# Performance work log

Measured on AMD Instinct MI355X. Metric: run time of the kernel, lower is better.

## Reference

```python
import jax, jax.numpy as jnp
import numpy as np

M_HIST = 5        # Anderson history depth (m=5 in anderson_solver)
N_POWER = 20      # power iterations to estimate sigma for spectral_norm
REG = 1e-4        # Tikhonov regularization on the Anderson LS system
MAX_ITER = 25     # deq_max_iter


def _l2norm(x):
    return x / (jnp.linalg.norm(x) + 1e-12)


def spectral_normalize(W):
    # torch spectral_norm: W / sigma, sigma = u^T W v with u,v from power iteration
    u = _l2norm(jnp.ones((W.shape[0],), W.dtype))
    def body(_, u):
        v = _l2norm(W.T @ u)
        return _l2norm(W @ v)
    u = jax.lax.fori_loop(0, N_POWER, body, u)
    v = _l2norm(W.T @ u)
    u = jax.lax.stop_gradient(u)
    v = jax.lax.stop_gradient(v)
    sigma = u @ (W @ v)
    return W / sigma


def make_f(W1, b1, W2, b2):
    W1s = spectral_normalize(W1)
    W2s = spectral_normalize(W2)
    def f(z, context):
        h = jnp.tanh(jnp.concatenate([z, context], axis=-1) @ W1s.T + b1)
        return jnp.tanh(h @ W2s.T + b2)
    return f


def anderson(f, x0, context, max_iter, m=M_HIST):
    # Mirrors anderson_solver, including its duplicated warm-up step.
    X = [x0]
    F = [f(x0, context)]
    x = F[0]; X.append(x); F.append(f(x, context))
    x = F[0]; X.append(x); F.append(f(x, context))
    for _k in range(2, max_iter):
        m_k = min(len(X) - 1, m)
        dX = jnp.stack([X[-i] - X[-i - 1] for i in range(1, m_k + 1)], axis=-1)  # [B,d,mk]
        dF = jnp.stack([F[-i] - F[-i - 1] for i in range(1, m_k + 1)], axis=-1)
        dG = dF - dX
        A = jnp.einsum('bdi,bdj->bij', dG, dG) + REG * jnp.eye(m_k, dtype=x0.dtype)
        r = F[-1] - X[-1]
        Bv = jnp.einsum('bdi,bd->bi', dG, r)
        alpha = jnp.linalg.solve(A, Bv[..., None])[..., 0]          # [B,mk]
        x = F[-1] - jnp.einsum('bdi,bi->bd', dF, alpha)
        X.append(x)
        F.append(f(x, context))
        if len(X) > m + 1:
            X.pop(0); F.pop(0)
    return X[-1]


def setup_inputs() -> dict:
    key = jax.random.key(0)
    ks = jax.random.split(key, 5)
    B, X_DIM, LATENT, HIDDEN = 2048, 256, 256, 1024
    context = jax.random.normal(ks[0], (B, X_DIM), jnp.float32)
    W1 = jax.random.normal(ks[1], (HIDDEN, LATENT + X_DIM), jnp.float32) / np.sqrt(LATENT + X_DIM)
    b1 = jax.random.normal(ks[2], (HIDDEN,), jnp.float32) * 0.01
    W2 = jax.random.normal(ks[3], (LATENT, HIDDEN), jnp.float32) / np.sqrt(HIDDEN)
    b2 = jax.random.normal(ks[4], (LATENT,), jnp.float32) * 0.01
    return {"context": context, "W1": W1, "b1": b1, "W2": W2, "b2": b2}


def reference(context, W1, b1, W2, b2):
    f = make_f(W1, b1, W2, b2)
    z0 = jnp.zeros((context.shape[0], W2.shape[0]), context.dtype)
    z_star = anderson(f, z0, context, MAX_ITER)
    return z_star
```

## Files before the change

### kernel.cpp

```cpp
#include <hip/hip_runtime.h>
#include <hip/hip_bf16.h>


#define B_ROWS 2048
#define D_LAT  256
#define D_CTX  256
#define D_HID  1024
#define KCAT   512
#define SLOT   (B_ROWS * D_LAT)
#define NRING  7

typedef __bf16 bf16x8 __attribute__((ext_vector_type(8)));
typedef float f32x4 __attribute__((ext_vector_type(4)));
typedef unsigned short u16;

__global__ void init_kernel(const float* __restrict__ ctx,
                            __hip_bfloat16* __restrict__ zc,
                            float* __restrict__ vA, float* __restrict__ uA,
                            float* __restrict__ G1p, float* __restrict__ G2) {
  int i = blockIdx.x * 256 + threadIdx.x;
  if (i < B_ROWS * KCAT) {
    int b = i >> 9, c = i & 511;
    float v = (c < 256) ? 0.0f : ctx[b * 256 + (c - 256)];
    zc[i] = __float2bfloat16(v);
  }
  if (i < 512 * 512) G1p[i] = 0.0f;
  if (i < 256 * 256) G2[i] = 0.0f;
  if (i < KCAT) vA[i] = 0.0f;
  if (i < D_LAT) uA[i] = 1.0f;
}

__global__ __launch_bounds__(256) void gram_kernel(
    const float* __restrict__ W1, const float* __restrict__ W2,
    float* __restrict__ G1p, float* __restrict__ G2) {
  __shared__ float As[32][66];
  __shared__ float Bs[32][34];
  const int tid = threadIdx.x;
  const int tx = tid & 15, ty = tid >> 4;

  const float* X; float* G; int N, ti, tj, k0base; bool modeA;
  int b = blockIdx.x;
  if (b < 1024) {
    modeA = true; X = W1; G = G1p; N = 512;
    int s = b >> 7, t = b & 127;
    ti = t >> 4; tj = t & 15; k0base = s * 128;
  } else {
    modeA = false; b -= 1024; X = W2; G = G2; N = 256;
    int s = b >> 5, t = b & 31;
    ti = t >> 3; tj = t & 7; k0base = s * 128;
  }

  float acc[4][2] = {};
  for (int k0 = k0base; k0 < k0base + 128; k0 += 32) {
    if (modeA) {
      for (int idx = tid; idx < 2048; idx += 256) {
        int r = idx & 63, c = idx >> 6;
        As[c][r] = X[(size_t)(k0 + c) * 512 + ti * 64 + r];
      }
      for (int idx = tid; idx < 1024; idx += 256) {
        int r = idx & 31, c = idx >> 5;
        Bs[c][r] = X[(size_t)(k0 + c) * 512 + tj * 32 + r];
      }
    } else {
      for (int idx = tid; idx < 2048; idx += 256) {
        int c = idx & 31, r = idx >> 5;
        As[c][r] = X[(size_t)(ti * 64 + r) * 1024 + k0 + c];
      }
      for (int idx = tid; idx < 1024; idx += 256) {
        int c = idx & 31, r = idx >> 5;
        Bs[c][r] = X[(size_t)(tj * 32 + r) * 1024 + k0 + c];
      }
    }
    __syncthreads();
#pragma unroll
    for (int kk = 0; kk < 32; kk++) {
      const float2* ap = (const float2*)&As[kk][ty * 4];
      float2 a0 = ap[0], a1 = ap[1];
      float2 b0 = *(const float2*)&Bs[kk][tx * 2];
      float a[4] = {a0.x, a0.y, a1.x, a1.y};
      float bb[2] = {b0.x, b0.y};
#pragma unroll
      for (int i = 0; i < 4; i++)
#pragma unroll
        for (int j = 0; j < 2; j++) acc[i][j] += a[i] * bb[j];
    }
    __syncthreads();
  }
#pragma unroll
  for (int i = 0; i < 4; i++)
#pragma unroll
    for (int j = 0; j < 2; j++)
      atomicAdd(&G[(size_t)(ti * 64 + ty * 4 + i) * N + tj * 32 + tx * 2 + j],
                acc[i][j]);
}

__global__ __launch_bounds__(256) void colsum_kernel(
    const float* __restrict__ W1, float* __restrict__ vA) {
  int b = blockIdx.x;
  for (int c = threadIdx.x; c < KCAT; c += 256) {
    float s = 0.f;
#pragma unroll
    for (int r = 0; r < 16; r++) s += W1[(size_t)(16 * b + r) * KCAT + c];
    atomicAdd(&vA[c], s);
  }
}

__global__ __launch_bounds__(256) void pmv_kernel(
    const float* __restrict__ G1p, const float* __restrict__ G2,
    const float* __restrict__ vi, float* __restrict__ vo,
    const float* __restrict__ ui, float* __restrict__ uo, int g1_active) {
  int gw = blockIdx.x * 4 + (threadIdx.x >> 6);
  int lane = threadIdx.x & 63;
  const float* G; const float* in; float* out; int n, r;
  if (gw < 512) {
    if (!g1_active) return;
    G = G1p; in = vi; out = vo; n = 512; r = gw;
  } else {
    G = G2; in = ui; out = uo; n = 256; r = gw - 512;
  }
  const float4* Gr = (const float4*)(G + (size_t)r * n);
  const float4* uv = (const float4*)in;
  float acc = 0.f;
  for (int c = lane; c < (n >> 2); c += 64) {
    float4 g = Gr[c], u = uv[c];
    acc += g.x * u.x + g.y * u.y + g.z * u.z + g.w * u.w;
  }
  for (int off = 32; off; off >>= 1) acc += __shfl_down(acc, off, 64);
  if (lane == 0) out[r] = 0.25f * acc;
}

__global__ __launch_bounds__(256) void sigma_kernel(
    const float* __restrict__ vA, const float* __restrict__ vB,
    const float* __restrict__ uA, const float* __restrict__ uB,
    float* __restrict__ sig) {
  float s[4] = {0.f, 0.f, 0.f, 0.f};
  for (int i = threadIdx.x; i < KCAT; i += 256) {
    s[0] += vA[i] * vB[i];
    s[1] += vA[i] * vA[i];
  }
  for (int i = threadIdx.x; i < D_LAT; i += 256) {
    s[2] += uA[i] * uA[i];
    s[3] += uA[i] * uB[i];
  }
  __shared__ float red[4][4];
  int lane = threadIdx.x & 63, w = threadIdx.x >> 6;
  for (int k = 0; k < 4; k++) {
    float a = s[k];
    for (int off = 32; off; off >>= 1) a += __shfl_down(a, off, 64);
    if (lane == 0) red[k][w] = a;
  }
  __syncthreads();
  if (threadIdx.x == 0) {
    float d0 = red[0][0] + red[0][1] + red[0][2] + red[0][3];
    float d1 = red[1][0] + red[1][1] + red[1][2] + red[1][3];
    float d2 = red[2][0] + red[2][1] + red[2][2] + red[2][3];
    float d3 = red[3][0] + red[3][1] + red[3][2] + red[3][3];
    sig[0] = sqrtf(0.25f * d0 / d1);
    sig[1] = sqrtf(0.25f * d2 / d3);
  }
}

__global__ void wfold_kernel(const float* __restrict__ W1,
                             const float* __restrict__ W2,
                             const float* __restrict__ sig,
                             __hip_bfloat16* __restrict__ W1b,
                             __hip_bfloat16* __restrict__ W2b) {
  int i = blockIdx.x * 256 + threadIdx.x;
  if (i < D_HID * KCAT) W1b[i] = __float2bfloat16(W1[i] * sig[0]);
  int j = i - D_HID * KCAT;
  if (j >= 0 && j < D_LAT * D_HID) W2b[j] = __float2bfloat16(W2[j] * sig[1]);
}

__global__ void warm1_kernel(const float* __restrict__ Fh,
                             float* __restrict__ Xh,
                             __hip_bfloat16* __restrict__ zc) {
  int i = blockIdx.x * 256 + threadIdx.x;
  float v = Fh[i];
  Xh[SLOT + i] = v;
  zc[(i >> 8) * KCAT + (i & 255)] = __float2bfloat16(v);
}
__global__ void warm2_kernel(const float* __restrict__ Fh,
                             float* __restrict__ Xh, float* __restrict__ Fw) {
  int i = blockIdx.x * 256 + threadIdx.x;
  Xh[2 * SLOT + i] = Fh[i];
  Fw[2 * SLOT + i] = Fh[SLOT + i];
}

template <int BM, int BN, bool OUT_BF16>
__global__ __launch_bounds__(256) void gemm_mfma(
    const __hip_bfloat16* __restrict__ A, const __hip_bfloat16* __restrict__ W,
    int K, const float* __restrict__ bias, float* __restrict__ Cf,
    __hip_bfloat16* __restrict__ Cb, int N) {
  __shared__ __align__(16) u16 lds[(BM + BN) * 64];
  u16* As = lds;
  u16* Ws = lds + BM * 64;
  const int tid = threadIdx.x;
  const int lane = tid & 63;
  const int wid = tid >> 6;
  const int wy = wid >> 1, wx = wid & 1;
  constexpr int WM = BM / 2, WN = BN / 2;
  constexpr int MB = WM / 16, NB = WN / 16;
  const int bm = blockIdx.x * BM;
  const int bn = blockIdx.y * BN;
  const int rlo = lane & 15, quad = lane >> 4;

  f32x4 acc[MB][NB] = {};

  for (int k0 = 0; k0 < K; k0 += 64) {
    for (int c = tid; c < BM * 8; c += 256) {
      int r = c >> 3, o = (c & 7) ^ (r & 7);
      __builtin_amdgcn_global_load_lds(
          (const __attribute__((address_space(1))) void*)(A + (size_t)(bm + r) * K + k0 + o * 8),
          (__attribute__((address_space(3))) void*)(As + c * 8), 16, 0, 0);
    }
    for (int c = tid; c < BN * 8; c += 256) {
      int r = c >> 3, o = (c & 7) ^ (r & 7);
      __builtin_amdgcn_global_load_lds(
          (const __attribute__((address_space(1))) void*)(W + (size_t)(bn + r) * K + k0 + o * 8),
          (__attribute__((address_space(3))) void*)(Ws + c * 8), 16, 0, 0);
    }
    __syncthreads();
#pragma unroll
    for (int kk = 0; kk < 2; kk++) {
      bf16x8 af[MB], bfr[NB];
#pragma unroll
      for (int mb = 0; mb < MB; mb++) {
        int r = wy * WM + mb * 16 + rlo;
        int o = (kk * 4 + quad) ^ (r & 7);
        af[mb] = *(const bf16x8*)(As + (r * 8 + o) * 8);
      }
#pragma unroll
      for (int nb = 0; nb < NB; nb++) {
        int r = wx * WN + nb * 16 + rlo;
        int o = (kk * 4 + quad) ^ (r & 7);
        bfr[nb] = *(const bf16x8*)(Ws + (r * 8 + o) * 8);
      }
#pragma unroll
      for (int mb = 0; mb < MB; mb++)
#pragma unroll
        for (int nb = 0; nb < NB; nb++)
          acc[mb][nb] = __builtin_amdgcn_mfma_f32_16x16x32_bf16(
              af[mb], bfr[nb], acc[mb][nb], 0, 0, 0);
    }
    __syncthreads();
  }

#pragma unroll
  for (int mb = 0; mb < MB; mb++) {
#pragma unroll
    for (int nb = 0; nb < NB; nb++) {
      int n = bn + wx * WN + nb * 16 + rlo;
      float bv = bias[n];
#pragma unroll
      for (int rg = 0; rg < 4; rg++) {
        int m = bm + wy * WM + mb * 16 + quad * 4 + rg;
        float val = tanhf(acc[mb][nb][rg] + bv);
        if constexpr (OUT_BF16) {
          Cb[(size_t)m * N + n] = __float2bfloat16(val);
        } else {
          Cf[(size_t)m * N + n] = val;
        }
      }
    }
  }
}

template <int MK>
__global__ __launch_bounds__(256) void anderson_step_kernel(
    const float* __restrict__ Xh, const float* __restrict__ Fh,
    float* __restrict__ Xw, __hip_bfloat16* __restrict__ zc, int t) {
  const int lane = threadIdx.x & 63;
  const int wid = threadIdx.x >> 6;
  const int b = blockIdx.x * 4 + wid;
  const int base = b * D_LAT + 4 * lane;

  const int sl0 = (t - 1) % NRING;
  f32x4 fa = *(const f32x4*)(Fh + (size_t)sl0 * SLOT + base);
  f32x4 xa = *(const f32x4*)(Xh + (size_t)sl0 * SLOT + base);
  const f32x4 Fm1 = fa;
  const f32x4 r = fa - xa;

  f32x4 dF[MK], dG[MK];
#pragma unroll
  for (int i = 1; i <= MK; i++) {
    int s2 = (t - 1 - i) % NRING;
    f32x4 fb = *(const f32x4*)(Fh + (size_t)s2 * SLOT + base);
    f32x4 xb = *(const f32x4*)(Xh + (size_t)s2 * SLOT + base);
    dF[i - 1] = fa - fb;
    dG[i - 1] = dF[i - 1] - (xa - xb);
    fa = fb;
    xa = xb;
  }

  constexpr int NV = MK * (MK + 1) / 2 + MK;
  float vals[NV];
  {
    int p = 0;
#pragma unroll
    for (int i = 0; i < MK; i++)
#pragma unroll
      for (int j = i; j < MK; j++) {
        f32x4 q = dG[i] * dG[j];
        vals[p++] = q[0] + q[1] + q[2] + q[3];
      }
#pragma unroll
    for (int i = 0; i < MK; i++) {
      f32x4 q = dG[i] * r;
      vals[p++] = q[0] + q[1] + q[2] + q[3];
    }
  }
#pragma unroll
  for (int off = 1; off <= 32; off <<= 1)
#pragma unroll
    for (int v = 0; v < NV; v++) vals[v] += __shfl_xor(vals[v], off, 64);

  double A[MK][MK], bv[MK], alpha[MK];
  {
    int p = 0;
#pragma unroll
    for (int i = 0; i < MK; i++)
#pragma unroll
      for (int j = i; j < MK; j++) {
        A[i][j] = (double)vals[p];
        A[j][i] = (double)vals[p];
        p++;
      }
#pragma unroll
    for (int i = 0; i < MK; i++) A[i][i] += (double)1e-4f;
#pragma unroll
    for (int i = 0; i < MK; i++) bv[i] = (double)vals[p++];
  }

#pragma unroll
  for (int c = 0; c < MK; c++) {
    double inv = 1.0 / A[c][c];
#pragma unroll
    for (int rr = c + 1; rr < MK; rr++) {
      double fct = A[rr][c] * inv;
#pragma unroll
      for (int cc = c; cc < MK; cc++) A[rr][cc] -= fct * A[c][cc];
      bv[rr] -= fct * bv[c];
    }
  }
#pragma unroll
  for (int i = MK - 1; i >= 0; i--) {
    double s = bv[i];
#pragma unroll
    for (int j = i + 1; j < MK; j++) s -= A[i][j] * alpha[j];
    alpha[i] = s / A[i][i];
  }

  f32x4 x = Fm1;
#pragma unroll
  for (int i = 0; i < MK; i++) x -= dF[i] * (float)alpha[i];
  *(f32x4*)(Xw + base) = x;
  if (zc != nullptr) {
    union { __hip_bfloat16 h[4]; unsigned long long u; } cv;
#pragma unroll
    for (int j = 0; j < 4; j++) cv.h[j] = __float2bfloat16(x[j]);
    *(unsigned long long*)(zc + (size_t)b * KCAT + 4 * lane) = cv.u;
  }
}

static void eval_f(const __hip_bfloat16* zc, const __hip_bfloat16* W1b,
                   const __hip_bfloat16* W2b, const float* b1, const float* b2,
                   __hip_bfloat16* hb, float* Fout, hipStream_t stream) {
  gemm_mfma<64, 64, true><<<dim3(B_ROWS / 64, D_HID / 64), 256, 0, stream>>>(
      zc, W1b, KCAT, b1, nullptr, hb, D_HID);
  gemm_mfma<32, 32, false><<<dim3(B_ROWS / 32, D_LAT / 32), 256, 0, stream>>>(
      hb, W2b, D_HID, b2, Fout, nullptr, D_LAT);
}

extern "C" void kernel_launch(void* const* d_in, const int* in_sizes, int n_in,
                              void* d_out, int out_size, void* d_ws,
                              size_t ws_size, hipStream_t stream) {
  const float* ctx = (const float*)d_in[0];
  const float* W1 = (const float*)d_in[1];
  const float* b1 = (const float*)d_in[2];
  const float* W2 = (const float*)d_in[3];
  const float* b2 = (const float*)d_in[4];
  float* out = (float*)d_out;

  float* ws = (float*)d_ws;
  float* sig = ws;
  float* vA = ws + 16;
  float* vB = vA + KCAT;
  float* uA = vB + KCAT;
  float* uB = uA + D_LAT;
  float* G1p = uB + D_LAT;
  float* G2 = G1p + KCAT * KCAT;
  float* Xh = G2 + D_LAT * D_LAT;
  float* Fh = Xh + NRING * SLOT;
  __hip_bfloat16* W1b = (__hip_bfloat16*)(Fh + NRING * SLOT);
  __hip_bfloat16* W2b = W1b + D_HID * KCAT;
  __hip_bfloat16* zc = W2b + D_LAT * D_HID;
  __hip_bfloat16* hb = zc + B_ROWS * KCAT;

  init_kernel<<<(B_ROWS * KCAT + 255) / 256, 256, 0, stream>>>(ctx, zc, vA, uA,
                                                               G1p, G2);
  gram_kernel<<<1280, 256, 0, stream>>>(W1, W2, G1p, G2);
  colsum_kernel<<<64, 256, 0, stream>>>(W1, vA);

  for (int it = 1; it <= 21; it++) {
    const float* vi; float* vo;
    const float* ui; float* uo;
    if (it & 1) { vi = vB; vo = vA; ui = uA; uo = uB; }
    else        { vi = vA; vo = vB; ui = uB; uo = uA; }
    pmv_kernel<<<192, 256, 0, stream>>>(G1p, G2, vi, vo, ui, uo, it >= 2);
  }
  sigma_kernel<<<1, 256, 0, stream>>>(vA, vB, uA, uB, sig);
  wfold_kernel<<<(D_HID * KCAT + D_LAT * D_HID + 255) / 256, 256, 0, stream>>>(
      W1, W2, sig, W1b, W2b);

  hipMemsetAsync(Xh, 0, SLOT * sizeof(float), stream);

  eval_f(zc, W1b, W2b, b1, b2, hb, Fh, stream);
  warm1_kernel<<<SLOT / 256, 256, 0, stream>>>(Fh, Xh, zc);
  eval_f(zc, W1b, W2b, b1, b2, hb, Fh + SLOT, stream);
  warm2_kernel<<<SLOT / 256, 256, 0, stream>>>(Fh, Xh, Fh);

  for (int t = 3; t <= 25; t++) {
    int mk = (t - 1 < 5) ? (t - 1) : 5;
    float* Xw = (t == 25) ? out : (Xh + (t % NRING) * SLOT);
    __hip_bfloat16* zarg = (t == 25) ? nullptr : zc;
    dim3 g(B_ROWS / 4);
    if (mk == 2)
      anderson_step_kernel<2><<<g, 256, 0, stream>>>(Xh, Fh, Xw, zarg, t);
    else if (mk == 3)
      anderson_step_kernel<3><<<g, 256, 0, stream>>>(Xh, Fh, Xw, zarg, t);
    else if (mk == 4)
      anderson_step_kernel<4><<<g, 256, 0, stream>>>(Xh, Fh, Xw, zarg, t);
    else
      anderson_step_kernel<5><<<g, 256, 0, stream>>>(Xh, Fh, Xw, zarg, t);
    if (t < 25) {
      eval_f(zc, W1b, W2b, b1, b2, hb, Fh + (t % NRING) * SLOT, stream);
    }
  }
}
```

Before: 812.9 us.

## Fuse second GEMM with Anderson mixing step and merge colsum into gram kernel

Adds a kernel that computes the second GEMM (hidden to latent, with tanh) for 16-row tiles covering the full latent width and then does the Anderson least-squares solve and mixing update for those rows in the same block. This removes one kernel launch per iteration and the round trip of F through global memory before the Anderson step. The least-squares solve now runs in float instead of double. Separately, the column-sum power-iteration seed is folded into the gram kernel as extra blocks, saving one more launch. The cost is lower GEMM parallelism (128 blocks of 512 threads), which may leave compute units idle.

```diff
diff --git a/kernel.cpp b/kernel.cpp
--- a/kernel.cpp
+++ b/kernel.cpp
@@ -32,14 +32,26 @@
 
 __global__ __launch_bounds__(256) void gram_kernel(
     const float* __restrict__ W1, const float* __restrict__ W2,
-    float* __restrict__ G1p, float* __restrict__ G2) {
+    float* __restrict__ G1p, float* __restrict__ G2,
+    float* __restrict__ vA) {
   __shared__ float As[32][66];
   __shared__ float Bs[32][34];
   const int tid = threadIdx.x;
   const int tx = tid & 15, ty = tid >> 4;
 
+  int b = blockIdx.x;
+  if (b >= 1280) {
+    int cb = b - 1280;
+    for (int c = tid; c < KCAT; c += 256) {
+      float s = 0.f;
+#pragma unroll
+      for (int r = 0; r < 16; r++) s += W1[(size_t)(16 * cb + r) * KCAT + c];
+      atomicAdd(&vA[c], s);
+    }
+    return;
+  }
+
   const float* X; float* G; int N, ti, tj, k0base; bool modeA;
-  int b = blockIdx.x;
   if (b < 1024) {
     modeA = true; X = W1; G = G1p; N = 512;
     int s = b >> 7, t = b & 127;
@@ -92,17 +104,6 @@
     for (int j = 0; j < 2; j++)
       atomicAdd(&G[(size_t)(ti * 64 + ty * 4 + i) * N + tj * 32 + tx * 2 + j],
                 acc[i][j]);
-}
-
-__global__ __launch_bounds__(256) void colsum_kernel(
-    const float* __restrict__ W1, float* __restrict__ vA) {
-  int b = blockIdx.x;
-  for (int c = threadIdx.x; c < KCAT; c += 256) {
-    float s = 0.f;
-#pragma unroll
-    for (int r = 0; r < 16; r++) s += W1[(size_t)(16 * b + r) * KCAT + c];
-    atomicAdd(&vA[c], s);
-  }
 }
 
 __global__ __launch_bounds__(256) void pmv_kernel(
@@ -362,6 +363,160 @@
   }
 }
 
+template <int MK, bool LAST>
+__global__ __launch_bounds__(512, 4) void gemm2_anderson_kernel(
+    const __hip_bfloat16* __restrict__ hb, const __hip_bfloat16* __restrict__ W2b,
+    const float* __restrict__ b2, float* __restrict__ Fh,
+    float* __restrict__ Xh, float* __restrict__ Xw,
+    __hip_bfloat16* __restrict__ zc, int t) {
+  __shared__ __align__(16) u16 lds[(16 + 256) * 64];
+  __shared__ __align__(16) float Fs[16][272];
+  u16* As = lds;
+  u16* Ws = lds + 16 * 64;
+  const int tid = threadIdx.x;
+  const int lane = tid & 63;
+  const int w = tid >> 6;
+  const int rlo = lane & 15, quad = lane >> 4;
+  const int bm = blockIdx.x * 16;
+
+  f32x4 acc[2] = {};
+  for (int k0 = 0; k0 < 1024; k0 += 64) {
+    if (tid < 128) {
+      int r = tid >> 3, o = (tid & 7) ^ (r & 7);
+      __builtin_amdgcn_global_load_lds(
+          (const __attribute__((address_space(1))) void*)(hb + (size_t)(bm + r) * 1024 + k0 + o * 8),
+          (__attribute__((address_space(3))) void*)(As + tid * 8), 16, 0, 0);
+    }
+    for (int c = tid; c < 2048; c += 512) {
+      int r = c >> 3, o = (c & 7) ^ (r & 7);
+      __builtin_amdgcn_global_load_lds(
+          (const __attribute__((address_space(1))) void*)(W2b + (size_t)r * 1024 + k0 + o * 8),
+          (__attribute__((address_space(3))) void*)(Ws + c * 8), 16, 0, 0);
+    }
+    __syncthreads();
+#pragma unroll
+    for (int kk = 0; kk < 2; kk++) {
+      int oa = (kk * 4 + quad) ^ (rlo & 7);
+      bf16x8 af = *(const bf16x8*)(As + (rlo * 8 + oa) * 8);
+#pragma unroll
+      for (int nb = 0; nb < 2; nb++) {
+        int r2 = 32 * w + nb * 16 + rlo;
+        int ob = (kk * 4 + quad) ^ (r2 & 7);
+        bf16x8 bf = *(const bf16x8*)(Ws + (r2 * 8 + ob) * 8);
+        acc[nb] = __builtin_amdgcn_mfma_f32_16x16x32_bf16(af, bf, acc[nb], 0, 0, 0);
+      }
+    }
+    __syncthreads();
+  }
+
+  float* Fout = Fh + (size_t)((t - 1) % NRING) * SLOT;
+#pragma unroll
+  for (int nb = 0; nb < 2; nb++) {
+    int n = 32 * w + nb * 16 + rlo;
+    float bvv = b2[n];
+#pragma unroll
+    for (int rg = 0; rg < 4; rg++) {
+      int m = quad * 4 + rg;
+      float val = tanhf(acc[nb][rg] + bvv);
+      Fout[(size_t)(bm + m) * 256 + n] = val;
+      Fs[m][n] = val;
+    }
+  }
+  __syncthreads();
+
+#pragma unroll 1
+  for (int rr = 0; rr < 2; rr++) {
+    const int row = 2 * w + rr;
+    const int base = (bm + row) * D_LAT + 4 * lane;
+
+    f32x4 fa = *(const f32x4*)&Fs[row][4 * lane];
+    const f32x4 Fm1 = fa;
+    f32x4 xa = *(const f32x4*)(Xh + (size_t)((t - 1) % NRING) * SLOT + base);
+    const f32x4 r = fa - xa;
+
+    f32x4 dF[MK], dG[MK];
+#pragma unroll
+    for (int i = 1; i <= MK; i++) {
+      int s2 = (t - 1 - i) % NRING;
+      f32x4 fb = *(const f32x4*)(Fh + (size_t)s2 * SLOT + base);
+      f32x4 xb = *(const f32x4*)(Xh + (size_t)s2 * SLOT + base);
+      dF[i - 1] = fa - fb;
+      dG[i - 1] = dF[i - 1] - (xa - xb);
+      fa = fb;
+      xa = xb;
+    }
+
+    constexpr int NV = MK * (MK + 1) / 2 + MK;
+    float vals[NV];
+    {
+      int p = 0;
+#pragma unroll
+      for (int i = 0; i < MK; i++)
+#pragma unroll
+        for (int j = i; j < MK; j++) {
+          f32x4 q = dG[i] * dG[j];
+          vals[p++] = q[0] + q[1] + q[2] + q[3];
+        }
+#pragma unroll
+      for (int i = 0; i < MK; i++) {
+        f32x4 q = dG[i] * r;
+        vals[p++] = q[0] + q[1] + q[2] + q[3];
+      }
+    }
+#pragma unroll
+    for (int off = 1; off <= 32; off <<= 1)
+#pragma unroll
+      for (int v = 0; v < NV; v++) vals[v] += __shfl_xor(vals[v], off, 64);
+
+    float A[MK][MK], bv[MK], alpha[MK];
+    {
+      int p = 0;
+#pragma unroll
+      for (int i = 0; i < MK; i++)
+#pragma unroll
+        for (int j = i; j < MK; j++) {
+          A[i][j] = vals[p];
+          A[j][i] = vals[p];
+          p++;
+        }
+#pragma unroll
+      for (int i = 0; i < MK; i++) A[i][i] += 1e-4f;
+#pragma unroll
+      for (int i = 0; i < MK; i++) bv[i] = vals[p++];
+    }
+
+#pragma unroll
+    for (int c = 0; c < MK; c++) {
+      float inv = 1.0f / A[c][c];
+#pragma unroll
+      for (int r2 = c + 1; r2 < MK; r2++) {
+        float fct = A[r2][c] * inv;
+#pragma unroll
+        for (int cc = c; cc < MK; cc++) A[r2][cc] -= fct * A[c][cc];
+        bv[r2] -= fct * bv[c];
+      }
+    }
+#pragma unroll
+    for (int i = MK - 1; i >= 0; i--) {
+      float s = bv[i];
+#pragma unroll
+      for (int j = i + 1; j < MK; j++) s -= A[i][j] * alpha[j];
+      alpha[i] = s / A[i][i];
+    }
+
+    f32x4 x = Fm1;
+#pragma unroll
+    for (int i = 0; i < MK; i++) x -= dF[i] * alpha[i];
+    *(f32x4*)(Xw + base) = x;
+    if constexpr (!LAST) {
+      union { __hip_bfloat16 h[4]; unsigned long long u; } cv;
+#pragma unroll
+      for (int j = 0; j < 4; j++) cv.h[j] = __float2bfloat16(x[j]);
+      *(unsigned long long*)(zc + (size_t)(bm + row) * KCAT + 4 * lane) = cv.u;
+    }
+  }
+}
+
 static void eval_f(const __hip_bfloat16* zc, const __hip_bfloat16* W1b,
                    const __hip_bfloat16* W2b, const float* b1, const float* b2,
                    __hip_bfloat16* hb, float* Fout, hipStream_t stream) {
@@ -398,8 +553,7 @@
 
   init_kernel<<<(B_ROWS * KCAT + 255) / 256, 256, 0, stream>>>(ctx, zc, vA, uA,
                                                                G1p, G2);
-  gram_kernel<<<1280, 256, 0, stream>>>(W1, W2, G1p, G2);
-  colsum_kernel<<<64, 256, 0, stream>>>(W1, vA);
+  gram_kernel<<<1344, 256, 0, stream>>>(W1, W2, G1p, G2, vA);
 
   for (int it = 1; it <= 21; it++) {
     const float* vi; float* vo;
@@ -418,22 +572,27 @@
   warm1_kernel<<<SLOT / 256, 256, 0, stream>>>(Fh, Xh, zc);
   eval_f(zc, W1b, W2b, b1, b2, hb, Fh + SLOT, stream);
   warm2_kernel<<<SLOT / 256, 256, 0, stream>>>(Fh, Xh, Fh);
-
-  for (int t = 3; t <= 25; t++) {
-    int mk = (t - 1 < 5) ? (t - 1) : 5;
-    float* Xw = (t == 25) ? out : (Xh + (t % NRING) * SLOT);
-    __hip_bfloat16* zarg = (t == 25) ? nullptr : zc;
-    dim3 g(B_ROWS / 4);
-    if (mk == 2)
-      anderson_step_kernel<2><<<g, 256, 0, stream>>>(Xh, Fh, Xw, zarg, t);
+  anderson_step_kernel<2><<<B_ROWS / 4, 256, 0, stream>>>(
+      Xh, Fh, Xh + (3 % NRING) * SLOT, zc, 3);
+
+  for (int t = 3; t <= 24; t++) {
+    gemm_mfma<64, 64, true><<<dim3(B_ROWS / 64, D_HID / 64), 256, 0, stream>>>(
+        zc, W1b, KCAT, b1, nullptr, hb, D_HID);
+    int tn = t + 1;
+    int mk = (tn - 1 < 5) ? tn - 1 : 5;
+    float* Xw = (tn == 25) ? out : (Xh + (tn % NRING) * SLOT);
+    dim3 g(B_ROWS / 16);
+    if (tn == 25)
+      gemm2_anderson_kernel<5, true><<<g, 512, 0, stream>>>(
+          hb, W2b, b2, Fh, Xh, Xw, nullptr, tn);
     else if (mk == 3)
-      anderson_step_kernel<3><<<g, 256, 0, stream>>>(Xh, Fh, Xw, zarg, t);
+      gemm2_anderson_kernel<3, false><<<g, 512, 0, stream>>>(
+          hb, W2b, b2, Fh, Xh, Xw, zc, tn);
     else if (mk == 4)
-      anderson_step_kernel<4><<<g, 256, 0, stream>>>(Xh, Fh, Xw, zarg, t);
+      gemm2_anderson_kernel<4, false><<<g, 512, 0, stream>>>(
+          hb, W2b, b2, Fh, Xh, Xw, zc, tn);
     else
-      anderson_step_kernel<5><<<g, 256, 0, stream>>>(Xh, Fh, Xw, zarg, t);
-    if (t < 25) {
-      eval_f(zc, W1b, W2b, b1, b2, hb, Fh + (t % NRING) * SLOT, stream);
-    }
-  }
-}
+      gemm2_anderson_kernel<5, false><<<g, 512, 0, stream>>>(
+          hb, W2b, b2, Fh, Xh, Xw, zc, tn);
+  }
+}
```

Result: slower. 996.5 us (+22.6%).

## Split Anderson rows across two waves, solve in fp32, fuse colsum into gram

Applied to the files above, without the earlier changes.

The Anderson step now assigns two wavefronts per batch row, each covering half of the latent dimension with float2 loads, and combines their partial dot products through shared memory. The small linear solve switches from double to float to avoid slow FP64 arithmetic. The column-sum kernel is folded into the gram kernel as extra blocks, which saves one launch. Together these should raise parallelism and cut latency in the many per-iteration Anderson launches, at the cost of a block-wide sync and reduced solve precision.

```diff
diff --git a/kernel.cpp b/kernel.cpp
--- a/kernel.cpp
+++ b/kernel.cpp
@@ -12,6 +12,7 @@
 
 typedef __bf16 bf16x8 __attribute__((ext_vector_type(8)));
 typedef float f32x4 __attribute__((ext_vector_type(4)));
+typedef float f32x2 __attribute__((ext_vector_type(2)));
 typedef unsigned short u16;
 
 __global__ void init_kernel(const float* __restrict__ ctx,
@@ -32,14 +33,26 @@
 
 __global__ __launch_bounds__(256) void gram_kernel(
     const float* __restrict__ W1, const float* __restrict__ W2,
-    float* __restrict__ G1p, float* __restrict__ G2) {
+    float* __restrict__ G1p, float* __restrict__ G2,
+    float* __restrict__ vA) {
   __shared__ float As[32][66];
   __shared__ float Bs[32][34];
   const int tid = threadIdx.x;
   const int tx = tid & 15, ty = tid >> 4;
 
+  int b = blockIdx.x;
+  if (b >= 1280) {
+    int cb = b - 1280;
+    for (int c = tid; c < KCAT; c += 256) {
+      float s = 0.f;
+#pragma unroll
+      for (int r = 0; r < 16; r++) s += W1[(size_t)(16 * cb + r) * KCAT + c];
+      atomicAdd(&vA[c], s);
+    }
+    return;
+  }
+
   const float* X; float* G; int N, ti, tj, k0base; bool modeA;
-  int b = blockIdx.x;
   if (b < 1024) {
     modeA = true; X = W1; G = G1p; N = 512;
     int s = b >> 7, t = b & 127;
@@ -92,17 +105,6 @@
     for (int j = 0; j < 2; j++)
       atomicAdd(&G[(size_t)(ti * 64 + ty * 4 + i) * N + tj * 32 + tx * 2 + j],
                 acc[i][j]);
-}
-
-__global__ __launch_bounds__(256) void colsum_kernel(
-    const float* __restrict__ W1, float* __restrict__ vA) {
-  int b = blockIdx.x;
-  for (int c = threadIdx.x; c < KCAT; c += 256) {
-    float s = 0.f;
-#pragma unroll
-    for (int r = 0; r < 16; r++) s += W1[(size_t)(16 * b + r) * KCAT + c];
-    atomicAdd(&vA[c], s);
-  }
 }
 
 __global__ __launch_bounds__(256) void pmv_kernel(
@@ -266,26 +268,27 @@
 }
 
 template <int MK>
-__global__ __launch_bounds__(256) void anderson_step_kernel(
+__global__ __launch_bounds__(256, 4) void anderson_step_kernel(
     const float* __restrict__ Xh, const float* __restrict__ Fh,
     float* __restrict__ Xw, __hip_bfloat16* __restrict__ zc, int t) {
   const int lane = threadIdx.x & 63;
-  const int wid = threadIdx.x >> 6;
-  const int b = blockIdx.x * 4 + wid;
-  const int base = b * D_LAT + 4 * lane;
+  const int w = threadIdx.x >> 6;
+  const int half = w & 1, rowi = w >> 1;
+  const int b = blockIdx.x * 2 + rowi;
+  const int base = b * D_LAT + half * 128 + 2 * lane;
 
   const int sl0 = (t - 1) % NRING;
-  f32x4 fa = *(const f32x4*)(Fh + (size_t)sl0 * SLOT + base);
-  f32x4 xa = *(const f32x4*)(Xh + (size_t)sl0 * SLOT + base);
-  const f32x4 Fm1 = fa;
-  const f32x4 r = fa - xa;
-
-  f32x4 dF[MK], dG[MK];
+  f32x2 fa = *(const f32x2*)(Fh + (size_t)sl0 * SLOT + base);
+  f32x2 xa = *(const f32x2*)(Xh + (size_t)sl0 * SLOT + base);
+  const f32x2 Fm1 = fa;
+  const f32x2 r = fa - xa;
+
+  f32x2 dF[MK], dG[MK];
 #pragma unroll
   for (int i = 1; i <= MK; i++) {
     int s2 = (t - 1 - i) % NRING;
-    f32x4 fb = *(const f32x4*)(Fh + (size_t)s2 * SLOT + base);
-    f32x4 xb = *(const f32x4*)(Xh + (size_t)s2 * SLOT + base);
+    f32x2 fb = *(const f32x2*)(Fh + (size_t)s2 * SLOT + base);
+    f32x2 xb = *(const f32x2*)(Xh + (size_t)s2 * SLOT + base);
     dF[i - 1] = fa - fb;
     dG[i - 1] = dF[i - 1] - (xa - xb);
     fa = fb;
@@ -300,13 +303,13 @@
     for (int i = 0; i < MK; i++)
 #pragma unroll
       for (int j = i; j < MK; j++) {
-        f32x4 q = dG[i] * dG[j];
-        vals[p++] = q[0] + q[1] + q[2] + q[3];
+        f32x2 q = dG[i] * dG[j];
+        vals[p++] = q[0] + q[1];
       }
 #pragma unroll
     for (int i = 0; i < MK; i++) {
-      f32x4 q = dG[i] * r;
-      vals[p++] = q[0] + q[1] + q[2] + q[3];
+      f32x2 q = dG[i] * r;
+      vals[p++] = q[0] + q[1];
     }
   }
 #pragma unroll
@@ -314,29 +317,38 @@
 #pragma unroll
     for (int v = 0; v < NV; v++) vals[v] += __shfl_xor(vals[v], off, 64);
 
-  double A[MK][MK], bv[MK], alpha[MK];
+  __shared__ float lv[2][2][NV];
+  if (lane == 0) {
+#pragma unroll
+    for (int v = 0; v < NV; v++) lv[rowi][half][v] = vals[v];
+  }
+  __syncthreads();
+#pragma unroll
+  for (int v = 0; v < NV; v++) vals[v] = lv[rowi][0][v] + lv[rowi][1][v];
+
+  float A[MK][MK], bv[MK], alpha[MK];
   {
     int p = 0;
 #pragma unroll
     for (int i = 0; i < MK; i++)
 #pragma unroll
       for (int j = i; j < MK; j++) {
-        A[i][j] = (double)vals[p];
-        A[j][i] = (double)vals[p];
+        A[i][j] = vals[p];
+        A[j][i] = vals[p];
         p++;
       }
 #pragma unroll
-    for (int i = 0; i < MK; i++) A[i][i] += (double)1e-4f;
-#pragma unroll
-    for (int i = 0; i < MK; i++) bv[i] = (double)vals[p++];
+    for (int i = 0; i < MK; i++) A[i][i] += 1e-4f;
+#pragma unroll
+    for (int i = 0; i < MK; i++) bv[i] = vals[p++];
   }
 
 #pragma unroll
   for (int c = 0; c < MK; c++) {
-    double inv = 1.0 / A[c][c];
+    float inv = 1.0f / A[c][c];
 #pragma unroll
     for (int rr = c + 1; rr < MK; rr++) {
-      double fct = A[rr][c] * inv;
+      float fct = A[rr][c] * inv;
 #pragma unroll
       for (int cc = c; cc < MK; cc++) A[rr][cc] -= fct * A[c][cc];
       bv[rr] -= fct * bv[c];
@@ -344,21 +356,21 @@
   }
 #pragma unroll
   for (int i = MK - 1; i >= 0; i--) {
-    double s = bv[i];
+    float s = bv[i];
 #pragma unroll
     for (int j = i + 1; j < MK; j++) s -= A[i][j] * alpha[j];
     alpha[i] = s / A[i][i];
   }
 
-  f32x4 x = Fm1;
-#pragma unroll
-  for (int i = 0; i < MK; i++) x -= dF[i] * (float)alpha[i];
-  *(f32x4*)(Xw + base) = x;
+  f32x2 x = Fm1;
+#pragma unroll
+  for (int i = 0; i < MK; i++) x -= dF[i] * alpha[i];
+  *(f32x2*)(Xw + base) = x;
   if (zc != nullptr) {
-    union { __hip_bfloat16 h[4]; unsigned long long u; } cv;
-#pragma unroll
-    for (int j = 0; j < 4; j++) cv.h[j] = __float2bfloat16(x[j]);
-    *(unsigned long long*)(zc + (size_t)b * KCAT + 4 * lane) = cv.u;
+    union { __hip_bfloat16 h[2]; unsigned int u; } cv;
+    cv.h[0] = __float2bfloat16(x[0]);
+    cv.h[1] = __float2bfloat16(x[1]);
+    *(unsigned int*)(zc + (size_t)b * KCAT + half * 128 + 2 * lane) = cv.u;
   }
 }
 
@@ -398,8 +410,7 @@
 
   init_kernel<<<(B_ROWS * KCAT + 255) / 256, 256, 0, stream>>>(ctx, zc, vA, uA,
                                                                G1p, G2);
-  gram_kernel<<<1280, 256, 0, stream>>>(W1, W2, G1p, G2);
-  colsum_kernel<<<64, 256, 0, stream>>>(W1, vA);
+  gram_kernel<<<1344, 256, 0, stream>>>(W1, W2, G1p, G2, vA);
 
   for (int it = 1; it <= 21; it++) {
     const float* vi; float* vo;
@@ -423,7 +434,7 @@
     int mk = (t - 1 < 5) ? (t - 1) : 5;
     float* Xw = (t == 25) ? out : (Xh + (t % NRING) * SLOT);
     __hip_bfloat16* zarg = (t == 25) ? nullptr : zc;
-    dim3 g(B_ROWS / 4);
+    dim3 g(B_ROWS / 2);
     if (mk == 2)
       anderson_step_kernel<2><<<g, 256, 0, stream>>>(Xh, Fh, Xw, zarg, t);
     else if (mk == 3)
```

New measurement: 874.1 us. 7.5% more time.
